# Kernel optimization log

Hardware: AMD Instinct MI355X
Metric: run time of the kernel (lower is better)

## Reference

```python
import jax, jax.numpy as jnp
import numpy as np

K_BITS = 8
D_V = 32

# 256-entry popcount lookup table (float, matching torch buffer)
_POP_LUT = jnp.asarray(np.array([bin(i).count('1') for i in range(256)], dtype=np.float32))


def setup_inputs() -> dict:
    key = jax.random.key(0)
    k1, k2, k3 = jax.random.split(key, 3)
    B, H, W = 8, 64, 64
    z = jax.random.uniform(k1, (B, K_BITS, H, W), dtype=jnp.float32)
    temperature = jnp.asarray(1.0, dtype=jnp.float32)
    value_embed = jax.random.normal(k2, (256, D_V), dtype=jnp.float32)  # nn.Embedding default N(0,1)
    return {"z": z, "temperature": temperature, "value_embed": value_embed}


def reference(z, temperature, value_embed):
    B, k, H, W = z.shape
    N = H * W
    d_v = value_embed.shape[1]
    # bitpack: threshold to {0,1}, pack k bits into one byte code per position
    bits = (z > 0.5).astype(jnp.int32)                       # (B,k,H,W)
    shifts = (2 ** jnp.arange(k, dtype=jnp.int32)).reshape(1, k, 1, 1)
    codes = (bits * shifts).sum(axis=1).reshape(B, N)        # (B,N) in [0,255]
    # pairwise Hamming distance via XOR + LUT popcount
    xor = codes[:, :, None] ^ codes[:, None, :]              # (B,N,N) int
    dist = _POP_LUT[xor]                                     # (B,N,N) float
    scores = -dist / jnp.clip(temperature, 0.1)
    attn = jax.nn.softmax(scores, axis=-1)                   # (B,N,N)
    values = value_embed[jnp.clip(codes, 0, 255)]            # (B,N,d_v)
    ctx = jnp.einsum('bnm,bmd->bnd', attn, values)           # (B,N,d_v)
    return ctx.transpose(0, 2, 1).reshape(B, d_v, H, W)
```

## Files before the change

kernel.cpp:

```cpp
#include <hip/hip_runtime.h>
#include <hip/hip_bf16.h>

#define B_SZ   8
#define KBITS  8
#define NPOS   4096
#define DV     32
#define NCODE  256
#define NSLICE 32

__global__ __launch_bounds__(1024) void k_fused(const float* __restrict__ z,
                                                const float* __restrict__ V,
                                                const float* __restrict__ temp,
                                                float* __restrict__ out) {
    const int b = blockIdx.x >> 5;
    const int s = blockIdx.x & (NSLICE - 1);
    const int tid = threadIdx.x;

    __shared__ unsigned int codes_u[NPOS / 4];
    __shared__ int h[NCODE];
    __shared__ float T[NCODE][DV + 1];

    if (tid < NCODE) h[tid] = 0;
    __syncthreads();

    {
        const float4* z4 = (const float4*)(z + (size_t)b * KBITS * NPOS);
        unsigned int c0 = 0, c1 = 0, c2 = 0, c3 = 0;
#pragma unroll
        for (int bit = 0; bit < KBITS; ++bit) {
            const float4 f = z4[bit * (NPOS / 4) + tid];
            c0 |= (unsigned)(f.x > 0.5f) << bit;
            c1 |= (unsigned)(f.y > 0.5f) << bit;
            c2 |= (unsigned)(f.z > 0.5f) << bit;
            c3 |= (unsigned)(f.w > 0.5f) << bit;
        }
        codes_u[tid] = c0 | (c1 << 8) | (c2 << 16) | (c3 << 24);
        atomicAdd(&h[c0], 1);
        atomicAdd(&h[c1], 1);
        atomicAdd(&h[c2], 1);
        atomicAdd(&h[c3], 1);
    }
    __syncthreads();

    for (int idx = tid; idx < NCODE * DV; idx += 1024) {
        const int v = idx >> 5, d = idx & 31;
        T[v][d] = (float)h[v] * V[v * DV + d];
    }
    if (tid < NCODE) T[tid][DV] = (float)h[tid];

    const float a = expf(-1.0f / fmaxf(temp[0], 0.1f));
#pragma unroll 1
    for (int st = 0; st < KBITS; ++st) {
        __syncthreads();
        for (int i = tid; i < (DV + 1) * 128; i += 1024) {
            const int c = i >> 7;
            const int p = i & 127;
            const int lo = p & ((1 << st) - 1);
            const int v0 = ((p >> st) << (st + 1)) | lo;
            const int v1 = v0 | (1 << st);
            const float t0 = T[v0][c], t1 = T[v1][c];
            T[v0][c] = fmaf(a, t1, t0);
            T[v1][c] = fmaf(a, t0, t1);
        }
    }
    __syncthreads();

    if (tid < NCODE) T[tid][DV] = 1.0f / T[tid][DV];
    __syncthreads();
    for (int idx = tid; idx < NCODE * DV; idx += 1024) {
        const int v = idx >> 5, d = idx & 31;
        T[v][d] *= T[v][DV];
    }
    __syncthreads();

    {
        const unsigned char* cbytes = (const unsigned char*)codes_u;
        const int nl = tid & 127;
        const int dg = tid >> 7;
        const int code = cbytes[s * 128 + nl];
        float* ob = out + (size_t)(b * DV) * NPOS + s * 128 + nl;
#pragma unroll
        for (int j = 0; j < 4; ++j) {
            const int d = dg + 8 * j;
            ob[(size_t)d * NPOS] = T[code][d];
        }
    }
}

extern "C" void kernel_launch(void* const* d_in, const int* in_sizes, int n_in,
                              void* d_out, int out_size, void* d_ws, size_t ws_size,
                              hipStream_t stream) {
    const float* z    = (const float*)d_in[0];
    const float* temp = (const float*)d_in[1];
    const float* V    = (const float*)d_in[2];
    float* out        = (float*)d_out;

    k_fused<<<B_SZ * NSLICE, 1024, 0, stream>>>(z, V, temp, out);
}
```

Measured before the change: 66.06 us.

## Move per-code butterfly transform into registers with wavefront shuffles

The 8-stage butterfly over the 256 code entries used to run in shared memory with a block barrier after each stage. It now runs in registers. Each thread holds 8 codes for one value dimension: the low 3 bits are combined in-thread and the high 5 bits through xor shuffles. The normalisation by the count is folded into the final shared-memory write, and the output scatter now uses uchar4 code loads with float4 stores. This removes most of the barriers and LDS traffic. In exchange it carries the count lane redundantly in every dimension's thread and uses the fast __expf.

```diff
diff --git a/kernel.cpp b/kernel.cpp
--- a/kernel.cpp
+++ b/kernel.cpp
@@ -12,13 +12,13 @@
                                                 const float* __restrict__ V,
                                                 const float* __restrict__ temp,
                                                 float* __restrict__ out) {
-    const int b = blockIdx.x >> 5;
-    const int s = blockIdx.x & (NSLICE - 1);
+    const int b   = blockIdx.x >> 5;
+    const int s   = blockIdx.x & (NSLICE - 1);
     const int tid = threadIdx.x;
 
     __shared__ unsigned int codes_u[NPOS / 4];
     __shared__ int h[NCODE];
-    __shared__ float T[NCODE][DV + 1];
+    __shared__ float T[NCODE * (DV + 1)];
 
     if (tid < NCODE) h[tid] = 0;
     __syncthreads();
@@ -42,48 +42,66 @@
     }
     __syncthreads();
 
-    for (int idx = tid; idx < NCODE * DV; idx += 1024) {
-        const int v = idx >> 5, d = idx & 31;
-        T[v][d] = (float)h[v] * V[v * DV + d];
+    const int d = tid >> 5;
+    const int l = tid & 31;
+    const float a = __expf(-1.0f / fmaxf(temp[0], 0.1f));
+
+    float val[8], cnt[8];
+#pragma unroll
+    for (int j = 0; j < 8; ++j) {
+        const int v = l * 8 + j;
+        const float c = (float)h[v];
+        cnt[j] = c;
+        val[j] = c * V[v * DV + d];
     }
-    if (tid < NCODE) T[tid][DV] = (float)h[tid];
 
-    const float a = expf(-1.0f / fmaxf(temp[0], 0.1f));
-#pragma unroll 1
-    for (int st = 0; st < KBITS; ++st) {
-        __syncthreads();
-        for (int i = tid; i < (DV + 1) * 128; i += 1024) {
-            const int c = i >> 7;
-            const int p = i & 127;
-            const int lo = p & ((1 << st) - 1);
-            const int v0 = ((p >> st) << (st + 1)) | lo;
-            const int v1 = v0 | (1 << st);
-            const float t0 = T[v0][c], t1 = T[v1][c];
-            T[v0][c] = fmaf(a, t1, t0);
-            T[v1][c] = fmaf(a, t0, t1);
+#pragma unroll
+    for (int st = 0; st < 3; ++st) {
+        const int m = 1 << st;
+#pragma unroll
+        for (int j = 0; j < 8; ++j) {
+            if ((j & m) == 0) {
+                const int j1 = j | m;
+                const float v0 = val[j], v1 = val[j1];
+                val[j]  = fmaf(a, v1, v0);
+                val[j1] = fmaf(a, v0, v1);
+                const float s0 = cnt[j], s1 = cnt[j1];
+                cnt[j]  = fmaf(a, s1, s0);
+                cnt[j1] = fmaf(a, s0, s1);
+            }
         }
     }
-    __syncthreads();
+#pragma unroll
+    for (int st = 0; st < 5; ++st) {
+        const int m = 1 << st;
+#pragma unroll
+        for (int j = 0; j < 8; ++j) {
+            const float pv = __shfl_xor(val[j], m);
+            val[j] = fmaf(a, pv, val[j]);
+            const float pc = __shfl_xor(cnt[j], m);
+            cnt[j] = fmaf(a, pc, cnt[j]);
+        }
+    }
 
-    if (tid < NCODE) T[tid][DV] = 1.0f / T[tid][DV];
-    __syncthreads();
-    for (int idx = tid; idx < NCODE * DV; idx += 1024) {
-        const int v = idx >> 5, d = idx & 31;
-        T[v][d] *= T[v][DV];
+#pragma unroll
+    for (int j = 0; j < 8; ++j) {
+        const int c = l * 8 + j;
+        T[c * (DV + 1) + d] = val[j] / cnt[j];
     }
     __syncthreads();
 
     {
-        const unsigned char* cbytes = (const unsigned char*)codes_u;
-        const int nl = tid & 127;
-        const int dg = tid >> 7;
-        const int code = cbytes[s * 128 + nl];
-        float* ob = out + (size_t)(b * DV) * NPOS + s * 128 + nl;
-#pragma unroll
-        for (int j = 0; j < 4; ++j) {
-            const int d = dg + 8 * j;
-            ob[(size_t)d * NPOS] = T[code][d];
-        }
+        const unsigned char* cb = (const unsigned char*)codes_u;
+        const int ng   = tid & 31;
+        const int base = s * 128 + ng * 4;
+        const uchar4 cc = *(const uchar4*)(cb + base);
+        float4 r;
+        r.x = T[cc.x * (DV + 1) + d];
+        r.y = T[cc.y * (DV + 1) + d];
+        r.z = T[cc.z * (DV + 1) + d];
+        r.w = T[cc.w * (DV + 1) + d];
+        float4* o4 = (float4*)(out + (size_t)(b * DV + d) * NPOS + base);
+        *o4 = r;
     }
 }
 
```

Measured after the change: 65.98 us. About the same (-0.1%).
